# Optimization experiments

Hardware: AMD Instinct MI355X
Metric: run time of the kernel (lower is better)

The kernel has to match this reference:

```python
import jax, jax.numpy as jnp
import numpy as np

LMBDA = 1000.0
GAMMA = 1.0  # resolvent_gamma


def setup_inputs() -> dict:
    key = jax.random.key(0)
    k = jax.random.split(key, 6)
    B, K, N, D = 16, 128, 8000, 256
    return {
        "evals_a": jax.random.uniform(k[0], (B, K), dtype=jnp.float32) + 1e-3,
        "pinv_a": jax.random.normal(k[1], (B, K, N), dtype=jnp.float32),
        "descr_a": jax.random.normal(k[2], (B, D, N), dtype=jnp.float32),
        "evals_b": jax.random.uniform(k[3], (B, K), dtype=jnp.float32) + 1e-3,
        "pinv_b": jax.random.normal(k[4], (B, K, N), dtype=jnp.float32),
        "descr_b": jax.random.normal(k[5], (B, D, N), dtype=jnp.float32),
    }


def _compute_mask(evals_a, evals_b, gamma):
    # evals_*: [B, K]. Per-batch normalization by joint max, then resolvent mask.
    scale = jnp.maximum(evals_a.max(axis=-1), evals_b.max(axis=-1))[:, None]
    ga = jnp.power(evals_a / scale, gamma)[:, None, :]  # [B, 1, K]
    gb = jnp.power(evals_b / scale, gamma)[:, :, None]  # [B, K, 1]
    M_re = gb / (gb * gb + 1.0) - ga / (ga * ga + 1.0)
    M_im = 1.0 / (gb * gb + 1.0) - 1.0 / (ga * ga + 1.0)
    return M_re * M_re + M_im * M_im  # [B, K, K]


def _compute_fmap(sdescr_a, sdescr_b, mask, lmbda):
    # sdescr_*: [B, D, K]; mask: [B, K, K]
    AA_aa = jnp.einsum("bdk,bdl->bkl", sdescr_a, sdescr_a)  # [B, K, K]
    AA_ba = jnp.einsum("bdk,bdl->bkl", sdescr_b, sdescr_a)  # [B, K, K]
    K = mask.shape[-1]
    eye = jnp.eye(K, dtype=mask.dtype)
    # Per row i: (AA_aa + lmbda * diag(mask[b, i, :]))^{-1} AA_ba[b, i, :]^T
    A = AA_aa[:, None, :, :] + lmbda * mask[..., None] * eye  # [B, K, K, K]
    Cab = jnp.linalg.solve(A, AA_ba[..., None])[..., 0]  # [B, K, K], row i = solution
    return Cab


def reference(evals_a, pinv_a, descr_a, evals_b, pinv_b, descr_b):
    # spectral descriptor projection: (pinv @ descr^T)^T -> [B, D, K]
    sdescr_a = jnp.einsum("bkn,bdn->bdk", pinv_a, descr_a)
    sdescr_b = jnp.einsum("bkn,bdn->bdk", pinv_b, descr_b)
    mask_ab = _compute_mask(evals_a, evals_b, GAMMA)
    fmap_12 = _compute_fmap(sdescr_a, sdescr_b, mask_ab, LMBDA)
    mask_ba = _compute_mask(evals_b, evals_a, GAMMA)
    fmap_21 = _compute_fmap(sdescr_b, sdescr_a, mask_ba, LMBDA)
    return (fmap_12, fmap_21)
```

## Files before the change

kernel.cpp:

```cpp
#include <hip/hip_runtime.h>

#define BB 16
#define KD 128
#define ND 8000
#define DD 256
#define LMB 1000.0f

typedef __attribute__((ext_vector_type(8))) short bf16x8;
typedef __attribute__((ext_vector_type(4))) short bf16x4;
typedef __attribute__((ext_vector_type(4))) float f32x4;
typedef unsigned short ushort_t;

__device__ __forceinline__ void split_bf16(float x, ushort_t& h, ushort_t& l) {
    unsigned int bi = __float_as_uint(x);
    h = (ushort_t)(bi >> 16);
    float lo = x - __uint_as_float(bi & 0xFFFF0000u);
    l = (ushort_t)(__float_as_uint(lo) >> 16);
}

__device__ __forceinline__ void split_bf16_rne(float x, ushort_t& h, ushort_t& l) {
    unsigned int bi = __float_as_uint(x);
    h = (ushort_t)(bi >> 16);
    float lo = x - __uint_as_float(bi & 0xFFFF0000u);
    unsigned int lb = __float_as_uint(lo);
    lb = lb + 0x7FFFu + ((lb >> 16) & 1u);
    l = (ushort_t)(lb >> 16);
}

__device__ __forceinline__ void cvt8(f32x4 a, f32x4 b, bf16x8& h, bf16x8& l) {
    #pragma unroll
    for (int j = 0; j < 4; ++j) {
        ushort_t hh, ll;
        split_bf16(a[j], hh, ll); h[j] = (short)hh; l[j] = (short)ll;
        split_bf16(b[j], hh, ll); h[4 + j] = (short)hh; l[4 + j] = (short)ll;
    }
}

__device__ __forceinline__ void gll16(const float* g, float* l) {
    __builtin_amdgcn_global_load_lds(
        (const __attribute__((address_space(1))) void*)g,
        (__attribute__((address_space(3))) void*)l, 16, 0, 0);
}

#define ROWS 384
#define CHF 32
#define NSL 8
#define SBUF_FL 12288
#define DEPTH 3

__global__ __attribute__((amdgpu_flat_work_group_size(1024, 1024)))
void proj_kernel(
    const float* __restrict__ pinv_a, const float* __restrict__ descr_a,
    const float* __restrict__ pinv_b, const float* __restrict__ descr_b,
    float* __restrict__ sd_a, float* __restrict__ sd_b)
{
    const int b = blockIdx.x, which = blockIdx.y, s = blockIdx.z;
    const float* P  = (which ? pinv_b  : pinv_a)  + (size_t)b * KD * ND;
    const float* Dm = (which ? descr_b : descr_a) + (size_t)b * DD * ND;
    float* outp = (which ? sd_b : sd_a) + (size_t)b * KD * DD;

    __shared__ float Sbuf[DEPTH][SBUF_FL];

    const int tid = threadIdx.x;
    const int lane = tid & 63;
    const int wid = tid >> 6;
    const int wm = wid >> 2, wn = wid & 3;
    const int fr = lane & 15;
    const int kg = lane >> 4;
    const int NC = (s < 2) ? 32 : 31;

    const float* gp[3];
    int lof[3];
    #pragma unroll
    for (int u = 0; u < 3; ++u) {
        int I = wid * 3 + u;
        int r = I * 8 + (lane >> 3);
        int c4 = (lane & 7) ^ (r & 7);
        const float* rowp = (r < KD) ? (P + (size_t)r * ND) : (Dm + (size_t)(r - KD) * ND);
        gp[u] = rowp + c4 * 4;
        lof[u] = I * 256;
    }

    f32x4 acc[2][4];
    #pragma unroll
    for (int i = 0; i < 2; ++i)
        #pragma unroll
        for (int j = 0; j < 4; ++j) acc[i][j] = (f32x4){0.f, 0.f, 0.f, 0.f};

    #pragma unroll
    for (int u = 0; u < 3; ++u) gll16(gp[u] + s * CHF, &Sbuf[0][lof[u]]);
    #pragma unroll
    for (int u = 0; u < 3; ++u) gll16(gp[u] + (s + NSL) * CHF, &Sbuf[1][lof[u]]);

    for (int t = 0; t < NC; ++t) {
        if (t + 2 < NC) {
            const int noff = (s + NSL * (t + 2)) * CHF;
            float* dst = &Sbuf[(t + 2) % DEPTH][0];
            #pragma unroll
            for (int u = 0; u < 3; ++u) gll16(gp[u] + noff, dst + lof[u]);
            __builtin_amdgcn_sched_barrier(0);
            asm volatile("s_waitcnt vmcnt(6)" ::: "memory");
        } else if (t + 1 < NC) {
            __builtin_amdgcn_sched_barrier(0);
            asm volatile("s_waitcnt vmcnt(3)" ::: "memory");
        } else {
            __builtin_amdgcn_sched_barrier(0);
            asm volatile("s_waitcnt vmcnt(0)" ::: "memory");
        }
        __builtin_amdgcn_sched_barrier(0);
        __builtin_amdgcn_s_barrier();
        __builtin_amdgcn_sched_barrier(0);

        const float* base = &Sbuf[t % DEPTH][0];

        bf16x8 Ah[2], Al[2];
        #pragma unroll
        for (int mi = 0; mi < 2; ++mi) {
            const int rA = wm * 32 + mi * 16 + fr;
            const int ra7 = rA & 7;
            f32x4 a0 = *(const f32x4*)(base + rA * CHF + (((2 * kg)     ^ ra7) << 2));
            f32x4 a1 = *(const f32x4*)(base + rA * CHF + (((2 * kg + 1) ^ ra7) << 2));
            cvt8(a0, a1, Ah[mi], Al[mi]);
        }
        #pragma unroll
        for (int ni = 0; ni < 4; ++ni) {
            const int rB = KD + wn * 64 + ni * 16 + fr;
            const int rb7 = rB & 7;
            f32x4 b0 = *(const f32x4*)(base + rB * CHF + (((2 * kg)     ^ rb7) << 2));
            f32x4 b1 = *(const f32x4*)(base + rB * CHF + (((2 * kg + 1) ^ rb7) << 2));
            bf16x8 Bh, Bl;
            cvt8(b0, b1, Bh, Bl);
            #pragma unroll
            for (int mi = 0; mi < 2; ++mi) {
                acc[mi][ni] = __builtin_amdgcn_mfma_f32_16x16x32_bf16(Ah[mi], Bh, acc[mi][ni], 0, 0, 0);
                acc[mi][ni] = __builtin_amdgcn_mfma_f32_16x16x32_bf16(Ah[mi], Bl, acc[mi][ni], 0, 0, 0);
                acc[mi][ni] = __builtin_amdgcn_mfma_f32_16x16x32_bf16(Al[mi], Bh, acc[mi][ni], 0, 0, 0);
            }
        }
        __builtin_amdgcn_sched_barrier(0);
        __builtin_amdgcn_s_barrier();
    }

    #pragma unroll
    for (int mi = 0; mi < 2; ++mi)
        #pragma unroll
        for (int ni = 0; ni < 4; ++ni) {
            int rbase = wm * 32 + mi * 16 + kg * 4;
            int ccol  = wn * 64 + ni * 16 + fr;
            #pragma unroll
            for (int r = 0; r < 4; ++r)
                atomicAdd(&outp[(size_t)(rbase + r) * DD + ccol], acc[mi][ni][r]);
        }
}

__global__ __launch_bounds__(256) void mask_kernel(
    const float* __restrict__ ea_g, const float* __restrict__ eb_g,
    float* __restrict__ lm_ab, float* __restrict__ lm_ba)
{
    const int b = blockIdx.x, tid = threadIdx.x;
    __shared__ float ta[KD], ua[KD], tb[KD], ub[KD];
    __shared__ float red[256];
    float e = (tid < KD) ? ea_g[b * KD + tid] : eb_g[b * KD + (tid - KD)];
    red[tid] = e;
    __syncthreads();
    for (int s = 128; s > 0; s >>= 1) {
        if (tid < s) red[tid] = fmaxf(red[tid], red[tid + s]);
        __syncthreads();
    }
    float is = 1.0f / red[0];
    float g = e * is;
    float den = 1.0f / (g * g + 1.0f);
    if (tid < KD) { ta[tid] = g * den; ua[tid] = den; }
    else          { tb[tid - KD] = g * den; ub[tid - KD] = den; }
    __syncthreads();
    for (int idx = tid; idx < KD * KD; idx += 256) {
        int i = idx >> 7, kc = idx & 127;
        float re = tb[i] - ta[kc], im = ub[i] - ua[kc];
        lm_ab[(size_t)b * KD * KD + idx] = LMB * (re * re + im * im);
        float re2 = ta[i] - tb[kc], im2 = ua[i] - ub[kc];
        lm_ba[(size_t)b * KD * KD + idx] = LMB * (re2 * re2 + im2 * im2);
    }
}

#define GSTR 68
__global__ __launch_bounds__(512, 2) void gram_kernel(
    const float* __restrict__ sd_a, const float* __restrict__ sd_b,
    float* __restrict__ AA)
{
    const int b = blockIdx.x, m = blockIdx.y, dchunk = blockIdx.z;
    const float* X = (m == 0) ? sd_a : sd_b;
    const float* Y = (m == 2) ? sd_a : X;
    X += (size_t)b * KD * DD;
    Y += (size_t)b * KD * DD;
    float* outp = AA + ((size_t)m * BB + b) * KD * KD;
    const int d0 = dchunk * 64;

    __shared__ ushort_t Xh[KD][GSTR], Xl[KD][GSTR];
    __shared__ ushort_t Yh[KD][GSTR], Yl[KD][GSTR];

    const int tid = threadIdx.x;
    const int lane = tid & 63;
    const int wid = tid >> 6;
    const int wm = wid >> 2, wn = wid & 3;
    const int fr = lane & 15;
    const int kg = lane >> 4;

    f32x4 acc[4][2];
    #pragma unroll
    for (int i = 0; i < 4; ++i)
        #pragma unroll
        for (int j = 0; j < 2; ++j) acc[i][j] = (f32x4){0.f, 0.f, 0.f, 0.f};

    #pragma unroll
    for (int u = 0; u < 8; ++u) {
        int idx = tid + (u & 3) * 512;
        int r = idx >> 4, c4 = idx & 15;
        const float* src = (u < 4) ? X : Y;
        float4 v = *(const float4*)(src + (size_t)r * DD + d0 + c4 * 4);
        float xs[4] = {v.x, v.y, v.z, v.w};
        bf16x4 hv, lv;
        #pragma unroll
        for (int q = 0; q < 4; ++q) {
            ushort_t hh, ll;
            split_bf16_rne(xs[q], hh, ll);
            hv[q] = (short)hh; lv[q] = (short)ll;
        }
        if (u < 4) {
            *(bf16x4*)&Xh[r][c4 * 4] = hv;
            *(bf16x4*)&Xl[r][c4 * 4] = lv;
        } else {
            *(bf16x4*)&Yh[r][c4 * 4] = hv;
            *(bf16x4*)&Yl[r][c4 * 4] = lv;
        }
    }
    __syncthreads();

    #pragma unroll
    for (int kk = 0; kk < 2; ++kk) {
        const int co = kk * 32 + kg * 8;
        bf16x8 Ah[4], Al[4];
        #pragma unroll
        for (int mi = 0; mi < 4; ++mi) {
            int r = wm * 64 + mi * 16 + fr;
            Ah[mi] = *(const bf16x8*)&Xh[r][co];
            Al[mi] = *(const bf16x8*)&Xl[r][co];
        }
        #pragma unroll
        for (int ni = 0; ni < 2; ++ni) {
            int c = wn * 32 + ni * 16 + fr;
            bf16x8 Bh = *(const bf16x8*)&Yh[c][co];
            bf16x8 Bl = *(const bf16x8*)&Yl[c][co];
            #pragma unroll
            for (int mi = 0; mi < 4; ++mi) {
                acc[mi][ni] = __builtin_amdgcn_mfma_f32_16x16x32_bf16(Ah[mi], Bh, acc[mi][ni], 0, 0, 0);
                acc[mi][ni] = __builtin_amdgcn_mfma_f32_16x16x32_bf16(Ah[mi], Bl, acc[mi][ni], 0, 0, 0);
                acc[mi][ni] = __builtin_amdgcn_mfma_f32_16x16x32_bf16(Al[mi], Bh, acc[mi][ni], 0, 0, 0);
            }
        }
    }

    #pragma unroll
    for (int mi = 0; mi < 4; ++mi)
        #pragma unroll
        for (int ni = 0; ni < 2; ++ni) {
            int rbase = wm * 64 + mi * 16 + kg * 4;
            int ccol  = wn * 32 + ni * 16 + fr;
            #pragma unroll
            for (int rr = 0; rr < 4; ++rr)
                atomicAdd(&outp[(size_t)(rbase + rr) * KD + ccol], acc[mi][ni][rr]);
        }
}

__global__ __launch_bounds__(512, 2) void invert_kernel(
    const float* __restrict__ AA, float* __restrict__ Hout)
{
    const int b = blockIdx.x, which = blockIdx.y;
    const float* src = AA + ((size_t)which * BB + b) * KD * KD;
    float* dst = Hout + ((size_t)which * BB + b) * KD * KD;

    __shared__ float rowbuf[2][KD];
    __shared__ float colbuf[2][KD];

    const int tid = threadIdx.x;
    const int rb = tid >> 5;
    const int cg = tid & 31;

    f32x4 Areg[8];
    #pragma unroll
    for (int r = 0; r < 8; ++r)
        Areg[r] = *(const f32x4*)(src + (size_t)(rb * 8 + r) * KD + cg * 4);

    if (rb == 0) *(f32x4*)&rowbuf[0][cg * 4] = Areg[0];
    if (cg == 0) {
        #pragma unroll
        for (int r = 0; r < 8; ++r) colbuf[0][rb * 8 + r] = Areg[r].x;
    }
    __syncthreads();

    for (int j = 0; j < KD; ++j) {
        const int cur = j & 1, nxt = cur ^ 1;
        const int jrb = j >> 3, jr = j & 7, jcg = j >> 2, jc = j & 3;
        const float pv = 1.0f / rowbuf[cur][j];
        const f32x4 orow = *(const f32x4*)&rowbuf[cur][cg * 4];
        const f32x4 prow = orow * pv;
        const bool mycg = (cg == jcg);
        const bool myrb = (rb == jrb);

        #pragma unroll
        for (int r = 0; r < 8; ++r) {
            const float cm = colbuf[cur][rb * 8 + r];
            const float cmul = -cm * pv;
            const bool piv = myrb && (r == jr);
            f32x4 nv;
            nv.x = piv ? prow.x : fmaf(cmul, orow.x, Areg[r].x);
            nv.y = piv ? prow.y : fmaf(cmul, orow.y, Areg[r].y);
            nv.z = piv ? prow.z : fmaf(cmul, orow.z, Areg[r].z);
            nv.w = piv ? prow.w : fmaf(cmul, orow.w, Areg[r].w);
            if (mycg) {
                const float fixv = piv ? pv : cmul;
                nv.x = (jc == 0) ? fixv : nv.x;
                nv.y = (jc == 1) ? fixv : nv.y;
                nv.z = (jc == 2) ? fixv : nv.z;
                nv.w = (jc == 3) ? fixv : nv.w;
            }
            Areg[r] = nv;
        }

        if (j + 1 < KD) {
            const int njrb = (j + 1) >> 3, njr = (j + 1) & 7;
            const int njcg = (j + 1) >> 2, njc = (j + 1) & 3;
            if (rb == njrb) {
                #pragma unroll
                for (int r = 0; r < 8; ++r)
                    if (r == njr) *(f32x4*)&rowbuf[nxt][cg * 4] = Areg[r];
            }
            if (cg == njcg) {
                #pragma unroll
                for (int r = 0; r < 8; ++r) {
                    const f32x4 a = Areg[r];
                    const float e = (njc == 0) ? a.x : (njc == 1) ? a.y : (njc == 2) ? a.z : a.w;
                    colbuf[nxt][rb * 8 + r] = e;
                }
            }
        }
        __syncthreads();
    }

    #pragma unroll
    for (int r = 0; r < 8; ++r)
        *(f32x4*)(dst + (size_t)(rb * 8 + r) * KD + cg * 4) = Areg[r];
}

#define NTERMS 4
__global__ __launch_bounds__(512) void solve_kernel(
    const float* __restrict__ AAba, const float* __restrict__ lm_ab,
    const float* __restrict__ lm_ba, const float* __restrict__ Hmat,
    float* __restrict__ outp)
{
    const int b = blockIdx.x, cg = blockIdx.y, which = blockIdx.z;
    const float* Hm = Hmat + ((size_t)which * BB + b) * KD * KD;
    const float* lm = (which ? lm_ba : lm_ab) + (size_t)b * KD * KD;
    const float* Rs = AAba + (size_t)b * KD * KD;
    float* op = outp + ((size_t)which * BB + b) * KD * KD;
    const int i0 = cg * 32;

    __shared__ float Hs[KD][132];
    __shared__ float Zc[2][32][132];
    __shared__ float lms[32][132];

    const int tid = threadIdx.x;
    const int rq = tid & 31;
    const int cq = tid >> 5;

    #pragma unroll
    for (int u = 0; u < 8; ++u) {
        int idx = tid + u * 512;
        int d = idx >> 5, l4 = idx & 31;
        *(float4*)&Hs[d][l4 * 4] = *(const float4*)(Hm + (size_t)d * KD + l4 * 4);
    }
    #pragma unroll
    for (int u = 0; u < 8; ++u) {
        int idx = tid + u * 512;
        int ic = idx >> 7, l = idx & 127;
        lms[ic][l] = lm[(size_t)(i0 + ic) * KD + l];
    }
    if (which == 0) {
        #pragma unroll
        for (int u = 0; u < 8; ++u) {
            int idx = tid + u * 512;
            int ic = idx >> 7, d = idx & 127;
            Zc[0][ic][d] = Rs[(size_t)(i0 + ic) * KD + d];
        }
    } else {
        #pragma unroll
        for (int u = 0; u < 8; ++u) {
            int idx = tid + u * 512;
            int d = idx >> 5, ic = idx & 31;
            Zc[0][ic][d] = Rs[(size_t)d * KD + i0 + ic];
        }
    }
    __syncthreads();

    float xacc[4][2];
    #pragma unroll
    for (int rr = 0; rr < 4; ++rr) { xacc[rr][0] = 0.f; xacc[rr][1] = 0.f; }
    int cur = 0;
    for (int t = 0; t < NTERMS; ++t) {
        float zr[4][2];
        #pragma unroll
        for (int rr = 0; rr < 4; ++rr) { zr[rr][0] = 0.f; zr[rr][1] = 0.f; }
        #pragma unroll 8
        for (int d4 = 0; d4 < 32; ++d4) {
            float4 hv[4];
            #pragma unroll
            for (int dd = 0; dd < 4; ++dd)
                hv[dd] = *(const float4*)&Hs[d4 * 4 + dd][rq * 4];
            float4 wv[2];
            #pragma unroll
            for (int cc = 0; cc < 2; ++cc)
                wv[cc] = *(const float4*)&Zc[cur][cq * 2 + cc][d4 * 4];
            #pragma unroll
            for (int cc = 0; cc < 2; ++cc) {
                zr[0][cc] += hv[0].x * wv[cc].x + hv[1].x * wv[cc].y + hv[2].x * wv[cc].z + hv[3].x * wv[cc].w;
                zr[1][cc] += hv[0].y * wv[cc].x + hv[1].y * wv[cc].y + hv[2].y * wv[cc].z + hv[3].y * wv[cc].w;
                zr[2][cc] += hv[0].z * wv[cc].x + hv[1].z * wv[cc].y + hv[2].z * wv[cc].z + hv[3].z * wv[cc].w;
                zr[3][cc] += hv[0].w * wv[cc].x + hv[1].w * wv[cc].y + hv[2].w * wv[cc].z + hv[3].w * wv[cc].w;
            }
        }
        const float s = (t & 1) ? -1.f : 1.f;
        #pragma unroll
        for (int rr = 0; rr < 4; ++rr) {
            xacc[rr][0] += s * zr[rr][0];
            xacc[rr][1] += s * zr[rr][1];
        }
        if (t + 1 < NTERMS) {
            #pragma unroll
            for (int cc = 0; cc < 2; ++cc) {
                float4 lmv = *(const float4*)&lms[cq * 2 + cc][rq * 4];
                float4 w;
                w.x = lmv.x * zr[0][cc];
                w.y = lmv.y * zr[1][cc];
                w.z = lmv.z * zr[2][cc];
                w.w = lmv.w * zr[3][cc];
                *(float4*)&Zc[cur ^ 1][cq * 2 + cc][rq * 4] = w;
            }
            __syncthreads();
            cur ^= 1;
        }
    }
    #pragma unroll
    for (int cc = 0; cc < 2; ++cc) {
        float4 o;
        o.x = xacc[0][cc]; o.y = xacc[1][cc]; o.z = xacc[2][cc]; o.w = xacc[3][cc];
        *(float4*)(op + (size_t)(i0 + cq * 2 + cc) * KD + rq * 4) = o;
    }
}

extern "C" void kernel_launch(void* const* d_in, const int* in_sizes, int n_in,
                              void* d_out, int out_size, void* d_ws, size_t ws_size,
                              hipStream_t stream) {
    (void)in_sizes; (void)n_in; (void)out_size; (void)ws_size;
    const float* evals_a = (const float*)d_in[0];
    const float* pinv_a  = (const float*)d_in[1];
    const float* descr_a = (const float*)d_in[2];
    const float* evals_b = (const float*)d_in[3];
    const float* pinv_b  = (const float*)d_in[4];
    const float* descr_b = (const float*)d_in[5];
    float* out = (float*)d_out;
    float* ws = (float*)d_ws;

    const size_t SD = (size_t)BB * KD * DD;
    const size_t MM = (size_t)BB * KD * KD;
    float* sd_a  = ws;
    float* sd_b  = sd_a + SD;
    float* AA    = sd_b + SD;
    float* lm_ab = AA + 3 * MM;
    float* lm_ba = lm_ab + MM;
    float* Hm    = lm_ba + MM;

    hipMemsetAsync(sd_a, 0, (2 * SD + 3 * MM) * sizeof(float), stream);
    proj_kernel<<<dim3(BB, 2, NSL), 1024, 0, stream>>>(pinv_a, descr_a, pinv_b, descr_b, sd_a, sd_b);
    mask_kernel<<<dim3(BB), 256, 0, stream>>>(evals_a, evals_b, lm_ab, lm_ba);
    gram_kernel<<<dim3(BB, 3, 4), 512, 0, stream>>>(sd_a, sd_b, AA);
    invert_kernel<<<dim3(BB, 2), 512, 0, stream>>>(AA, Hm);
    solve_kernel<<<dim3(BB, 4, 2), 512, 0, stream>>>(AA + 2 * MM, lm_ab, lm_ba, Hm, out);
}
```

Before: 280.1 us.

## Fuse mask computation into solve kernel and use split-bf16 MFMA for series

Removes the separate mask kernel and its global lm_ab/lm_ba buffers; each solve block recomputes its slice of the resolvent mask from the eigenvalues in shared memory. The Neumann-series matrix products in the solve kernel move from FP32 FMA loops to bf16 hi/lo split MFMA (three products per tile). This saves one launch and global mask traffic, and makes the series matmuls cheaper. The cost is a small per-block reduction and some precision loss from dropping the lo*lo term.

```diff
diff --git a/kernel.cpp b/kernel.cpp
--- a/kernel.cpp
+++ b/kernel.cpp
@@ -151,35 +151,6 @@
             for (int r = 0; r < 4; ++r)
                 atomicAdd(&outp[(size_t)(rbase + r) * DD + ccol], acc[mi][ni][r]);
         }
-}
-
-__global__ __launch_bounds__(256) void mask_kernel(
-    const float* __restrict__ ea_g, const float* __restrict__ eb_g,
-    float* __restrict__ lm_ab, float* __restrict__ lm_ba)
-{
-    const int b = blockIdx.x, tid = threadIdx.x;
-    __shared__ float ta[KD], ua[KD], tb[KD], ub[KD];
-    __shared__ float red[256];
-    float e = (tid < KD) ? ea_g[b * KD + tid] : eb_g[b * KD + (tid - KD)];
-    red[tid] = e;
-    __syncthreads();
-    for (int s = 128; s > 0; s >>= 1) {
-        if (tid < s) red[tid] = fmaxf(red[tid], red[tid + s]);
-        __syncthreads();
-    }
-    float is = 1.0f / red[0];
-    float g = e * is;
-    float den = 1.0f / (g * g + 1.0f);
-    if (tid < KD) { ta[tid] = g * den; ua[tid] = den; }
-    else          { tb[tid - KD] = g * den; ub[tid - KD] = den; }
-    __syncthreads();
-    for (int idx = tid; idx < KD * KD; idx += 256) {
-        int i = idx >> 7, kc = idx & 127;
-        float re = tb[i] - ta[kc], im = ub[i] - ua[kc];
-        lm_ab[(size_t)b * KD * KD + idx] = LMB * (re * re + im * im);
-        float re2 = ta[i] - tb[kc], im2 = ua[i] - ub[kc];
-        lm_ba[(size_t)b * KD * KD + idx] = LMB * (re2 * re2 + im2 * im2);
-    }
 }
 
 #define GSTR 68
@@ -352,107 +323,165 @@
 }
 
 #define NTERMS 4
+#define HSTR 136
 __global__ __launch_bounds__(512) void solve_kernel(
-    const float* __restrict__ AAba, const float* __restrict__ lm_ab,
-    const float* __restrict__ lm_ba, const float* __restrict__ Hmat,
+    const float* __restrict__ AAba, const float* __restrict__ ea_g,
+    const float* __restrict__ eb_g, const float* __restrict__ Hmat,
     float* __restrict__ outp)
 {
     const int b = blockIdx.x, cg = blockIdx.y, which = blockIdx.z;
     const float* Hm = Hmat + ((size_t)which * BB + b) * KD * KD;
-    const float* lm = (which ? lm_ba : lm_ab) + (size_t)b * KD * KD;
     const float* Rs = AAba + (size_t)b * KD * KD;
     float* op = outp + ((size_t)which * BB + b) * KD * KD;
     const int i0 = cg * 32;
 
-    __shared__ float Hs[KD][132];
-    __shared__ float Zc[2][32][132];
-    __shared__ float lms[32][132];
+    __shared__ ushort_t Hh[KD][HSTR], Hl[KD][HSTR];
+    __shared__ ushort_t Wh[32][HSTR], Wl[32][HSTR];
+    __shared__ float lmT[KD][33];
+    __shared__ float tC[KD], uC[KD], tR[32], uR[32];
+    __shared__ float red[256];
 
     const int tid = threadIdx.x;
-    const int rq = tid & 31;
-    const int cq = tid >> 5;
-
+    const int lane = tid & 63;
+    const int wid = tid >> 6;
+    const int wl = wid & 3, wi = wid >> 2;
+    const int fr = lane & 15;
+    const int kg = lane >> 4;
+
+    if (tid < 256) {
+        float e = (tid < KD) ? ea_g[b * KD + tid] : eb_g[b * KD + (tid - KD)];
+        red[tid] = e;
+    }
+    __syncthreads();
+    for (int s = 128; s > 0; s >>= 1) {
+        if (tid < s) red[tid] = fmaxf(red[tid], red[tid + s]);
+        __syncthreads();
+    }
+    const float is = 1.0f / red[0];
+    const float* Ce = which ? eb_g : ea_g;
+    const float* Re = which ? ea_g : eb_g;
+    if (tid < KD) {
+        float g = Ce[b * KD + tid] * is;
+        float den = 1.0f / (g * g + 1.0f);
+        tC[tid] = g * den; uC[tid] = den;
+    } else if (tid < KD + 32) {
+        int i = tid - KD;
+        float g = Re[b * KD + i0 + i] * is;
+        float den = 1.0f / (g * g + 1.0f);
+        tR[i] = g * den; uR[i] = den;
+    }
+    __syncthreads();
     #pragma unroll
     for (int u = 0; u < 8; ++u) {
         int idx = tid + u * 512;
-        int d = idx >> 5, l4 = idx & 31;
-        *(float4*)&Hs[d][l4 * 4] = *(const float4*)(Hm + (size_t)d * KD + l4 * 4);
-    }
+        int l = idx >> 5, i = idx & 31;
+        float re = tR[i] - tC[l], im = uR[i] - uC[l];
+        lmT[l][i] = LMB * (re * re + im * im);
+    }
+
     #pragma unroll
     for (int u = 0; u < 8; ++u) {
-        int idx = tid + u * 512;
-        int ic = idx >> 7, l = idx & 127;
-        lms[ic][l] = lm[(size_t)(i0 + ic) * KD + l];
+        int idx4 = (tid + u * 512) * 4;
+        int row = idx4 >> 7, col = idx4 & 127;
+        f32x4 v = *(const f32x4*)(Hm + (size_t)row * KD + col);
+        bf16x4 hv, lv;
+        #pragma unroll
+        for (int q = 0; q < 4; ++q) {
+            ushort_t hh, ll;
+            split_bf16(v[q], hh, ll);
+            hv[q] = (short)hh; lv[q] = (short)ll;
+        }
+        *(bf16x4*)&Hh[row][col] = hv;
+        *(bf16x4*)&Hl[row][col] = lv;
     }
     if (which == 0) {
+        #pragma unroll
+        for (int u = 0; u < 2; ++u) {
+            int idx4 = (tid + u * 512) * 4;
+            int i = idx4 >> 7, d = idx4 & 127;
+            f32x4 v = *(const f32x4*)(Rs + (size_t)(i0 + i) * KD + d);
+            bf16x4 hv, lv;
+            #pragma unroll
+            for (int q = 0; q < 4; ++q) {
+                ushort_t hh, ll;
+                split_bf16(v[q], hh, ll);
+                hv[q] = (short)hh; lv[q] = (short)ll;
+            }
+            *(bf16x4*)&Wh[i][d] = hv;
+            *(bf16x4*)&Wl[i][d] = lv;
+        }
+    } else {
         #pragma unroll
         for (int u = 0; u < 8; ++u) {
             int idx = tid + u * 512;
-            int ic = idx >> 7, d = idx & 127;
-            Zc[0][ic][d] = Rs[(size_t)(i0 + ic) * KD + d];
-        }
-    } else {
-        #pragma unroll
-        for (int u = 0; u < 8; ++u) {
-            int idx = tid + u * 512;
-            int d = idx >> 5, ic = idx & 31;
-            Zc[0][ic][d] = Rs[(size_t)d * KD + i0 + ic];
+            int i = idx & 31, d = idx >> 5;
+            float v = Rs[(size_t)d * KD + i0 + i];
+            ushort_t hh, ll;
+            split_bf16(v, hh, ll);
+            Wh[i][d] = hh; Wl[i][d] = ll;
         }
     }
     __syncthreads();
 
-    float xacc[4][2];
-    #pragma unroll
-    for (int rr = 0; rr < 4; ++rr) { xacc[rr][0] = 0.f; xacc[rr][1] = 0.f; }
-    int cur = 0;
+    f32x4 xacc[2];
+    xacc[0] = (f32x4){0.f, 0.f, 0.f, 0.f};
+    xacc[1] = (f32x4){0.f, 0.f, 0.f, 0.f};
+
     for (int t = 0; t < NTERMS; ++t) {
-        float zr[4][2];
-        #pragma unroll
-        for (int rr = 0; rr < 4; ++rr) { zr[rr][0] = 0.f; zr[rr][1] = 0.f; }
-        #pragma unroll 8
-        for (int d4 = 0; d4 < 32; ++d4) {
-            float4 hv[4];
-            #pragma unroll
-            for (int dd = 0; dd < 4; ++dd)
-                hv[dd] = *(const float4*)&Hs[d4 * 4 + dd][rq * 4];
-            float4 wv[2];
-            #pragma unroll
-            for (int cc = 0; cc < 2; ++cc)
-                wv[cc] = *(const float4*)&Zc[cur][cq * 2 + cc][d4 * 4];
-            #pragma unroll
-            for (int cc = 0; cc < 2; ++cc) {
-                zr[0][cc] += hv[0].x * wv[cc].x + hv[1].x * wv[cc].y + hv[2].x * wv[cc].z + hv[3].x * wv[cc].w;
-                zr[1][cc] += hv[0].y * wv[cc].x + hv[1].y * wv[cc].y + hv[2].y * wv[cc].z + hv[3].y * wv[cc].w;
-                zr[2][cc] += hv[0].z * wv[cc].x + hv[1].z * wv[cc].y + hv[2].z * wv[cc].z + hv[3].z * wv[cc].w;
-                zr[3][cc] += hv[0].w * wv[cc].x + hv[1].w * wv[cc].y + hv[2].w * wv[cc].z + hv[3].w * wv[cc].w;
-            }
-        }
-        const float s = (t & 1) ? -1.f : 1.f;
-        #pragma unroll
-        for (int rr = 0; rr < 4; ++rr) {
-            xacc[rr][0] += s * zr[rr][0];
-            xacc[rr][1] += s * zr[rr][1];
+        f32x4 az[2];
+        az[0] = (f32x4){0.f, 0.f, 0.f, 0.f};
+        az[1] = (f32x4){0.f, 0.f, 0.f, 0.f};
+        #pragma unroll
+        for (int kk = 0; kk < 4; ++kk) {
+            const int co = kk * 32 + kg * 8;
+            bf16x8 Bh = *(const bf16x8*)&Wh[wi * 16 + fr][co];
+            bf16x8 Bl = *(const bf16x8*)&Wl[wi * 16 + fr][co];
+            #pragma unroll
+            for (int mi = 0; mi < 2; ++mi) {
+                const int rA = wl * 32 + mi * 16 + fr;
+                bf16x8 Ah_ = *(const bf16x8*)&Hh[rA][co];
+                bf16x8 Al_ = *(const bf16x8*)&Hl[rA][co];
+                az[mi] = __builtin_amdgcn_mfma_f32_16x16x32_bf16(Ah_, Bh, az[mi], 0, 0, 0);
+                az[mi] = __builtin_amdgcn_mfma_f32_16x16x32_bf16(Ah_, Bl, az[mi], 0, 0, 0);
+                az[mi] = __builtin_amdgcn_mfma_f32_16x16x32_bf16(Al_, Bh, az[mi], 0, 0, 0);
+            }
+        }
+        const float sg = (t & 1) ? -1.f : 1.f;
+        #pragma unroll
+        for (int mi = 0; mi < 2; ++mi) {
+            xacc[mi][0] += sg * az[mi][0];
+            xacc[mi][1] += sg * az[mi][1];
+            xacc[mi][2] += sg * az[mi][2];
+            xacc[mi][3] += sg * az[mi][3];
         }
         if (t + 1 < NTERMS) {
-            #pragma unroll
-            for (int cc = 0; cc < 2; ++cc) {
-                float4 lmv = *(const float4*)&lms[cq * 2 + cc][rq * 4];
-                float4 w;
-                w.x = lmv.x * zr[0][cc];
-                w.y = lmv.y * zr[1][cc];
-                w.z = lmv.z * zr[2][cc];
-                w.w = lmv.w * zr[3][cc];
-                *(float4*)&Zc[cur ^ 1][cq * 2 + cc][rq * 4] = w;
-            }
             __syncthreads();
-            cur ^= 1;
-        }
-    }
-    #pragma unroll
-    for (int cc = 0; cc < 2; ++cc) {
+            const int i = wi * 16 + fr;
+            #pragma unroll
+            for (int mi = 0; mi < 2; ++mi) {
+                const int l0 = wl * 32 + mi * 16 + kg * 4;
+                bf16x4 hv, lv;
+                #pragma unroll
+                for (int r = 0; r < 4; ++r) {
+                    float w = lmT[l0 + r][i] * az[mi][r];
+                    ushort_t hh, ll;
+                    split_bf16(w, hh, ll);
+                    hv[r] = (short)hh; lv[r] = (short)ll;
+                }
+                *(bf16x4*)&Wh[i][l0] = hv;
+                *(bf16x4*)&Wl[i][l0] = lv;
+            }
+            __syncthreads();
+        }
+    }
+
+    const int i = wi * 16 + fr;
+    #pragma unroll
+    for (int mi = 0; mi < 2; ++mi) {
+        const int l0 = wl * 32 + mi * 16 + kg * 4;
         float4 o;
-        o.x = xacc[0][cc]; o.y = xacc[1][cc]; o.z = xacc[2][cc]; o.w = xacc[3][cc];
-        *(float4*)(op + (size_t)(i0 + cq * 2 + cc) * KD + rq * 4) = o;
+        o.x = xacc[mi][0]; o.y = xacc[mi][1]; o.z = xacc[mi][2]; o.w = xacc[mi][3];
+        *(float4*)(op + (size_t)(i0 + i) * KD + l0) = o;
     }
 }
 
@@ -474,14 +503,11 @@
     float* sd_a  = ws;
     float* sd_b  = sd_a + SD;
     float* AA    = sd_b + SD;
-    float* lm_ab = AA + 3 * MM;
-    float* lm_ba = lm_ab + MM;
-    float* Hm    = lm_ba + MM;
+    float* Hm    = AA + 3 * MM;
 
     hipMemsetAsync(sd_a, 0, (2 * SD + 3 * MM) * sizeof(float), stream);
     proj_kernel<<<dim3(BB, 2, NSL), 1024, 0, stream>>>(pinv_a, descr_a, pinv_b, descr_b, sd_a, sd_b);
-    mask_kernel<<<dim3(BB), 256, 0, stream>>>(evals_a, evals_b, lm_ab, lm_ba);
     gram_kernel<<<dim3(BB, 3, 4), 512, 0, stream>>>(sd_a, sd_b, AA);
     invert_kernel<<<dim3(BB, 2), 512, 0, stream>>>(AA, Hm);
-    solve_kernel<<<dim3(BB, 4, 2), 512, 0, stream>>>(AA + 2 * MM, lm_ab, lm_ba, Hm, out);
-}
+    solve_kernel<<<dim3(BB, 4, 2), 512, 0, stream>>>(AA + 2 * MM, evals_a, evals_b, Hm, out);
+}
```

Result: faster. 260.2 us (-7.1%).
